# Kernel optimization log

Hardware: AMD Instinct MI355X
Metric: run time of the kernel (lower is better)

The kernel has to match this reference:

```python
import jax, jax.numpy as jnp
import numpy as np


def _pe_2d(H, W, C, dtype):
    # PositionalEncodingPermute2D: returns (C, H, W)
    ch_half = (C + 1) // 2
    inv = 1.0 / (10000.0 ** (jnp.arange(0, ch_half, 2, dtype=jnp.float32) / ch_half))
    tH = jnp.arange(H, dtype=jnp.float32)
    tW = jnp.arange(W, dtype=jnp.float32)
    sinH = tH[:, None] * inv[None, :]              # (H, ch_half//2)
    sinW = tW[:, None] * inv[None, :]              # (W, ch_half//2)
    embH = jnp.concatenate([jnp.sin(sinH), jnp.cos(sinH)], axis=-1)  # (H, ch_half)
    embW = jnp.concatenate([jnp.sin(sinW), jnp.cos(sinW)], axis=-1)  # (W, ch_half)
    E = jnp.concatenate([
        jnp.broadcast_to(embW[None, :, :], (H, W, ch_half)),
        jnp.broadcast_to(embH[:, None, :], (H, W, ch_half)),
    ], axis=-1)[..., :C]                            # (H, W, C)
    return jnp.transpose(E, (2, 0, 1)).astype(dtype)  # (C, H, W)


def setup_inputs() -> dict:
    key = jax.random.key(0)
    k0, k1, k2, k3 = jax.random.split(key, 4)
    B, C, H, W = 4, 256, 64, 64
    s = 1.0 / np.sqrt(C)  # kaiming-ish scale
    return {
        "x": jax.random.normal(k0, (B, C, H, W), dtype=jnp.float32),
        "wq": jax.random.normal(k1, (C, C), dtype=jnp.float32) * s,
        "wk": jax.random.normal(k2, (C, C), dtype=jnp.float32) * s,
        "wv": jax.random.normal(k3, (C, C), dtype=jnp.float32) * s,
    }


def reference(x, wq, wk, wv):
    B, C, H, W = x.shape
    scale = C ** (-0.5)
    x = x + _pe_2d(H, W, C, x.dtype)[None]          # (B, C, H, W)
    X = x.reshape(B, C, H * W).transpose(0, 2, 1)   # (B, N, C)
    Q = jnp.einsum('bnc,dc->bnd', X, wq)
    K = jnp.einsum('bnc,dc->bnd', X, wk)
    V = jnp.einsum('bnc,dc->bnd', X, wv)
    A = jax.nn.softmax(jnp.einsum('bnd,bmd->bnm', Q, K) * scale, axis=-1)
    Y = jnp.einsum('bnm,bmd->bnd', A, V)            # (B, N, C)
    return Y.transpose(0, 2, 1).reshape(B, C, H, W)
```

## Files before the change

### kernel.cpp

```cpp
#include <hip/hip_runtime.h>
#include <hip/hip_bf16.h>

#define BB 4
#define CC 256
#define NN 4096
#define NSPLIT 4
#define KSPLIT (NN / NSPLIT)
#define NPAIR (KSPLIT / 64)

typedef __attribute__((ext_vector_type(8))) short short8;
typedef __attribute__((ext_vector_type(4))) float floatx4;
typedef __attribute__((ext_vector_type(4))) unsigned short ushortx4;

__device__ __forceinline__ float bf2f(unsigned short u) {
  union { unsigned int i; float f; } cv; cv.i = ((unsigned int)u) << 16; return cv.f;
}
__device__ __forceinline__ unsigned short f2bf(float f) {
  union { __hip_bfloat16 h; unsigned short u; } cv; cv.h = __float2bfloat16(f); return cv.u;
}
__device__ __forceinline__ unsigned int cvtpk_bf16(float lo, float hi) {
  unsigned int r;
  asm("v_cvt_pk_bf16_f32 %0, %1, %2" : "=v"(r) : "v"(lo), "v"(hi));
  return r;
}

#define MFMA(a, b, c) __builtin_amdgcn_mfma_f32_16x16x32_bf16((a), (b), (c), 0, 0, 0)

__device__ __forceinline__ void dma16(const unsigned short* g, unsigned short* l) {
  __builtin_amdgcn_global_load_lds(
      (const __attribute__((address_space(1))) unsigned int*)g,
      (__attribute__((address_space(3))) unsigned int*)l, 16, 0, 0);
}
#define S_BARRIER __builtin_amdgcn_s_barrier()
#define MEMFENCE __asm__ volatile("" ::: "memory")

__global__ __launch_bounds__(256) void wcvt(const float* __restrict__ w0,
                                            const float* __restrict__ w1,
                                            const float* __restrict__ w2,
                                            unsigned short* __restrict__ o0,
                                            unsigned short* __restrict__ o1,
                                            unsigned short* __restrict__ o2) {
  const float* w = (blockIdx.y == 0) ? w0 : (blockIdx.y == 1) ? w1 : w2;
  unsigned short* o = (blockIdx.y == 0) ? o0 : (blockIdx.y == 1) ? o1 : o2;
  float s = (blockIdx.y == 0) ? 0.0901684400555590f : 1.0f;
  int i = (blockIdx.x * 256 + threadIdx.x) * 4;
  floatx4 v = *(const floatx4*)&w[i];
  ushortx4 p;
#pragma unroll
  for (int r = 0; r < 4; r++) p[r] = f2bf(v[r] * s);
  *(ushortx4*)&o[i] = p;
}

__global__ __launch_bounds__(256) void prep_x(const float* __restrict__ x,
                                              unsigned short* __restrict__ Xbf) {
  __shared__ float tile[32][33];
  int b = blockIdx.z;
  int n0 = blockIdx.x * 32, c0 = blockIdx.y * 32;
  int tx = threadIdx.x, ty = threadIdx.y;
#pragma unroll
  for (int i = 0; i < 4; i++) {
    int c = c0 + ty + i * 8;
    int n = n0 + tx;
    float v = x[((long)(b * CC + c)) * NN + n];
    int hh = n >> 6, ww = n & 63;
    int j = c & 63;
    float freq = exp2f(-0.2076205059304601f * (float)j);
    float arg = (float)((c < 128) ? ww : hh) * freq;
    v += (c & 64) ? cosf(arg) : sinf(arg);
    tile[ty + i * 8][tx] = v;
  }
  __syncthreads();
#pragma unroll
  for (int i = 0; i < 4; i++) {
    int n = n0 + ty + i * 8;
    int c = c0 + tx;
    Xbf[((long)(b * NN + n)) * CC + c] = f2bf(tile[tx][ty + i * 8]);
  }
}

__global__ __launch_bounds__(256, 2) void gemm_fused(const unsigned short* __restrict__ Xbf,
                                                     const unsigned short* __restrict__ Wqk,
                                                     const unsigned short* __restrict__ Wv,
                                                     unsigned short* __restrict__ QK,
                                                     unsigned short* __restrict__ Vt) {
  __shared__ alignas(16) unsigned short Af[2][8 * 512];
  __shared__ alignas(16) unsigned short Bf[2][8 * 512];
  const unsigned short *Ab, *Bb;
  unsigned short* Ob;
  long row0, col0;
  int ldo;
  int F = blockIdx.x;
  if (F < 512) {
    int b = F >> 7, r = F & 127;
    row0 = (long)(r >> 2) * 128;
    col0 = (long)(r & 3) * 128;
    Ab = Xbf + (long)b * NN * CC;
    Bb = Wqk;
    Ob = QK + (long)b * NN * 512;
    ldo = 512;
  } else {
    int F2 = F - 512;
    int b = F2 >> 6, r = F2 & 63;
    row0 = (long)(r >> 5) * 128;
    col0 = (long)(r & 31) * 128;
    Ab = Wv;
    Bb = Xbf + (long)b * NN * CC;
    Ob = Vt + (long)b * CC * NN;
    ldo = NN;
  }
  int t = threadIdx.x, wave = t >> 6, lane = t & 63, quad = lane >> 4, l15 = lane & 15;
  int wr = wave >> 1, wc = wave & 1;

  auto stage = [&](int k0, int buf) {
#pragma unroll
    for (int i = 0; i < 2; i++) {
      int fg = wave * 2 + i;
      dma16(&Ab[(row0 + fg * 16 + l15) * 256 + k0 + quad * 8], &Af[buf][fg * 512]);
      dma16(&Bb[(col0 + fg * 16 + l15) * 256 + k0 + quad * 8], &Bf[buf][fg * 512]);
    }
  };

  floatx4 acc[4][4] = {};
  stage(0, 0);
  MEMFENCE;
#pragma unroll
  for (int ki = 0; ki < 8; ki++) {
    int buf = ki & 1;
    S_BARRIER;
    MEMFENCE;
    if (ki + 1 < 8) {
      stage((ki + 1) * 32, buf ^ 1);
      MEMFENCE;
      __builtin_amdgcn_s_waitcnt(0xF74);
    } else {
      __builtin_amdgcn_s_waitcnt(0xF70);
    }
    S_BARRIER;
    MEMFENCE;
    short8 af[4], bf[4];
#pragma unroll
    for (int i = 0; i < 4; i++) {
      af[i] = *(const short8*)&Af[buf][(wr * 4 + i) * 512 + lane * 8];
      bf[i] = *(const short8*)&Bf[buf][(wc * 4 + i) * 512 + lane * 8];
    }
#pragma unroll
    for (int i = 0; i < 4; i++)
#pragma unroll
      for (int j = 0; j < 4; j++) acc[i][j] = MFMA(af[i], bf[j], acc[i][j]);
  }

#pragma unroll
  for (int i = 0; i < 4; i++)
#pragma unroll
    for (int j = 0; j < 4; j++) {
      long col = col0 + (wc * 4 + j) * 16 + l15;
#pragma unroll
      for (int r = 0; r < 4; r++) {
        long row = row0 + (wr * 4 + i) * 16 + quad * 4 + r;
        Ob[row * (long)ldo + col] = f2bf(acc[i][j][r]);
      }
    }
}

__global__ __launch_bounds__(512, 2) void attn(const unsigned short* __restrict__ QKg,
                                               const unsigned short* __restrict__ Vtg,
                                               unsigned short* __restrict__ Opart,
                                               float* __restrict__ Lp) {
  __shared__ alignas(16) unsigned short Kl[4 * 8192];
  __shared__ alignas(16) unsigned short Vl[4 * 8192];
  int F = blockIdx.x;
  int c = F & 15, sp = c & 3, b = c >> 2;
  long q0 = (long)(F >> 4) * 256;
  int t = threadIdx.x, wave = t >> 6, lane = t & 63, quad = lane >> 4, l15 = lane & 15;
  const unsigned short* Qb = QKg + (long)b * NN * 512;
  const unsigned short* Kb = Qb + 256;
  const unsigned short* Vb = Vtg + (long)b * CC * NN;

  short8 qf[2][8];
#pragma unroll
  for (int qb = 0; qb < 2; qb++) {
    long qrow = q0 + wave * 32 + qb * 16 + l15;
#pragma unroll
    for (int ks = 0; ks < 8; ks++)
      qf[qb][ks] = *(const short8*)&Qb[qrow * 512 + ks * 32 + quad * 8];
  }

  floatx4 acc[2][16] = {};
  float rs[2] = {0.f, 0.f};

  const int idx0 = (((lane >> 4) & 1) << 7) | ((lane & 15) << 2);
  const int idx1 = idx0 + 64;
  const bool lo32 = lane < 32;

  const int kbeg = sp * KSPLIT;

  auto stage_pair = [&](int p, int buf) {
#pragma unroll
    for (int tt = 0; tt < 2; tt++) {
      int m0 = kbeg + (p * 2 + tt) * 32;
      int slot = buf * 2 + tt;
#pragma unroll
      for (int st = 0; st < 2; st++) {
        int fg = st * 8 + wave;
        dma16(&Kb[(long)(m0 + st * 16 + l15) * 512 + wave * 32 + quad * 8],
              &Kl[slot * 8192 + fg * 512]);
        dma16(&Vb[(long)(fg * 16 + l15) * NN + m0 + quad * 8],
              &Vl[slot * 8192 + fg * 512]);
      }
    }
  };

  __builtin_amdgcn_s_waitcnt(0xF70);
  stage_pair(0, 0);
  MEMFENCE;

  for (int p = 0; p < NPAIR; p++) {
    int buf = p & 1;
    S_BARRIER;
    MEMFENCE;
    if (p + 1 < NPAIR) {
      stage_pair(p + 1, buf ^ 1);
      MEMFENCE;
      __builtin_amdgcn_s_waitcnt(0xF78);
    } else {
      __builtin_amdgcn_s_waitcnt(0xF70);
    }
    S_BARRIER;
    MEMFENCE;

#pragma unroll
    for (int tt = 0; tt < 2; tt++) {
      int kb = (buf * 2 + tt) * 8192;
      floatx4 s2[2][2];
      {
        floatx4 z = {0.f, 0.f, 0.f, 0.f};
        s2[0][0] = z; s2[0][1] = z; s2[1][0] = z; s2[1][1] = z;
      }
      __builtin_amdgcn_s_setprio(1);
#pragma unroll
      for (int fgk = 0; fgk < 16; fgk++) {
        short8 kf = *(const short8*)&Kl[kb + fgk * 512 + lane * 8];
        int mt = fgk >> 3, ks = fgk & 7;
        s2[0][mt] = MFMA(kf, qf[0][ks], s2[0][mt]);
        s2[1][mt] = MFMA(kf, qf[1][ks], s2[1][mt]);
      }
      __builtin_amdgcn_s_setprio(0);

      unsigned int pw[2][2][2];
#pragma unroll
      for (int qb = 0; qb < 2; qb++)
#pragma unroll
        for (int mt = 0; mt < 2; mt++) {
          float e0 = __builtin_amdgcn_exp2f(s2[qb][mt][0]);
          float e1 = __builtin_amdgcn_exp2f(s2[qb][mt][1]);
          float e2 = __builtin_amdgcn_exp2f(s2[qb][mt][2]);
          float e3 = __builtin_amdgcn_exp2f(s2[qb][mt][3]);
          rs[qb] += (e0 + e1) + (e2 + e3);
          pw[qb][mt][0] = cvtpk_bf16(e0, e1);
          pw[qb][mt][1] = cvtpk_bf16(e2, e3);
        }

      short8 pf[2];
#pragma unroll
      for (int qb = 0; qb < 2; qb++) {
        unsigned int x0 = (unsigned int)__builtin_amdgcn_ds_bpermute(idx0, (int)pw[qb][0][0]);
        unsigned int y0 = (unsigned int)__builtin_amdgcn_ds_bpermute(idx0, (int)pw[qb][1][0]);
        unsigned int x1 = (unsigned int)__builtin_amdgcn_ds_bpermute(idx0, (int)pw[qb][0][1]);
        unsigned int y1 = (unsigned int)__builtin_amdgcn_ds_bpermute(idx0, (int)pw[qb][1][1]);
        unsigned int x2 = (unsigned int)__builtin_amdgcn_ds_bpermute(idx1, (int)pw[qb][0][0]);
        unsigned int y2 = (unsigned int)__builtin_amdgcn_ds_bpermute(idx1, (int)pw[qb][1][0]);
        unsigned int x3 = (unsigned int)__builtin_amdgcn_ds_bpermute(idx1, (int)pw[qb][0][1]);
        unsigned int y3 = (unsigned int)__builtin_amdgcn_ds_bpermute(idx1, (int)pw[qb][1][1]);
        union { unsigned int u[4]; short8 s; } pk;
        pk.u[0] = lo32 ? x0 : y0;
        pk.u[1] = lo32 ? x1 : y1;
        pk.u[2] = lo32 ? x2 : y2;
        pk.u[3] = lo32 ? x3 : y3;
        pf[qb] = pk.s;
      }

      __builtin_amdgcn_s_setprio(1);
#pragma unroll
      for (int db = 0; db < 16; db++) {
        short8 vf = *(const short8*)&Vl[kb + db * 512 + lane * 8];
        acc[0][db] = MFMA(pf[0], vf, acc[0][db]);
        acc[1][db] = MFMA(pf[1], vf, acc[1][db]);
      }
      __builtin_amdgcn_s_setprio(0);
    }
  }

  unsigned short* Ob = Opart + (long)(b * NSPLIT + sp) * CC * NN;
#pragma unroll
  for (int qb = 0; qb < 2; qb++) {
    long nidx = q0 + wave * 32 + qb * 16 + quad * 4;
#pragma unroll
    for (int db = 0; db < 16; db++) {
      long d = db * 16 + l15;
      ushortx4 pk;
#pragma unroll
      for (int r = 0; r < 4; r++) pk[r] = f2bf(acc[qb][db][r]);
      *(ushortx4*)&Ob[d * NN + nidx] = pk;
    }
    float v = rs[qb];
    v += __shfl_xor(v, 16, 64);
    v += __shfl_xor(v, 32, 64);
    if (quad == 0)
      Lp[(long)(b * NSPLIT + sp) * NN + q0 + wave * 32 + qb * 16 + l15] = v;
  }
}

__global__ __launch_bounds__(256) void combine(const unsigned short* __restrict__ Op,
                                               const float* __restrict__ Lp,
                                               float* __restrict__ Out) {
  __shared__ float Wl[64];
  int b = blockIdx.z;
  int d0 = blockIdx.y * 64, n0 = blockIdx.x * 64;
  int t = threadIdx.x;
  if (t < 64) {
    int n = n0 + t;
    float L = 0.f;
#pragma unroll
    for (int s = 0; s < NSPLIT; s++) L += Lp[(long)(b * NSPLIT + s) * NN + n];
    Wl[t] = 1.0f / L;
  }
  __syncthreads();
  int tn = t & 15, td = t >> 4;
  int nb = n0 + tn * 4;
  float w[4];
#pragma unroll
  for (int r = 0; r < 4; r++) w[r] = Wl[tn * 4 + r];
#pragma unroll
  for (int dd = 0; dd < 4; dd++) {
    int d = d0 + td * 4 + dd;
    floatx4 o = {0.f, 0.f, 0.f, 0.f};
#pragma unroll
    for (int s = 0; s < NSPLIT; s++) {
      ushortx4 pv = *(const ushortx4*)&Op[((long)(b * NSPLIT + s) * CC + d) * NN + nb];
#pragma unroll
      for (int r = 0; r < 4; r++) o[r] += bf2f(pv[r]);
    }
#pragma unroll
    for (int r = 0; r < 4; r++) o[r] *= w[r];
    *(floatx4*)&Out[((long)b * CC + d) * NN + nb] = o;
  }
}

extern "C" void kernel_launch(void* const* d_in, const int* in_sizes, int n_in,
                              void* d_out, int out_size, void* d_ws, size_t ws_size,
                              hipStream_t stream) {
  const float* x = (const float*)d_in[0];
  const float* wq = (const float*)d_in[1];
  const float* wk = (const float*)d_in[2];
  const float* wv = (const float*)d_in[3];
  float* out = (float*)d_out;

  char* ws = (char*)d_ws;
  unsigned short* QKbuf = (unsigned short*)(ws);
  unsigned short* Vt = (unsigned short*)(ws + (16l << 20));
  unsigned short* Xbf = (unsigned short*)(ws + (24l << 20));
  unsigned short* Opart = (unsigned short*)(ws + (24l << 20));
  float* Lp = (float*)(ws + (56l << 20));
  unsigned short* Wqk = (unsigned short*)(ws + (57l << 20));
  unsigned short* Wv = (unsigned short*)(ws + (57l << 20) + (1 << 19));

  wcvt<<<dim3(CC * CC / 1024, 3), 256, 0, stream>>>(wq, wk, wv, Wqk, Wqk + CC * CC, Wv);
  prep_x<<<dim3(NN / 32, CC / 32, BB), dim3(32, 8), 0, stream>>>(x, Xbf);
  gemm_fused<<<dim3(768), 256, 0, stream>>>(Xbf, Wqk, Wv, QKbuf, Vt);
  attn<<<dim3(256), 512, 0, stream>>>(QKbuf, Vt, Opart, Lp);
  combine<<<dim3(NN / 64, CC / 64, BB), 256, 0, stream>>>(Opart, Lp, out);
}
```

Before: 192.8 us.

## Halve attention query tile per block and double-buffer single key tiles

The attention kernel now gives each wave 16 query rows instead of 32, so a block covers 128 queries and the grid doubles to 512 blocks. It stages one 32-key tile at a time into a two-slot buffer instead of pairs of tiles into four slots, which halves LDS use and drops the min-blocks launch bound. The intent is to cut registers and LDS per block so more blocks fit per CU and latency is hidden better. In exchange, each K/V tile loaded into LDS is reused by half as many query rows, which doubles K/V global traffic and adds barrier overhead per key tile.

Result: slower. 240.0 us (+24.5%).

```diff
diff --git a/kernel.cpp b/kernel.cpp
--- a/kernel.cpp
+++ b/kernel.cpp
@@ -6,7 +6,7 @@
 #define NN 4096
 #define NSPLIT 4
 #define KSPLIT (NN / NSPLIT)
-#define NPAIR (KSPLIT / 64)
+#define NT (KSPLIT / 32)
 
 typedef __attribute__((ext_vector_type(8))) short short8;
 typedef __attribute__((ext_vector_type(4))) float floatx4;
@@ -162,31 +162,31 @@
     }
 }
 
-__global__ __launch_bounds__(512, 2) void attn(const unsigned short* __restrict__ QKg,
-                                               const unsigned short* __restrict__ Vtg,
-                                               unsigned short* __restrict__ Opart,
-                                               float* __restrict__ Lp) {
-  __shared__ alignas(16) unsigned short Kl[4 * 8192];
-  __shared__ alignas(16) unsigned short Vl[4 * 8192];
+__global__ __launch_bounds__(512) void attn(const unsigned short* __restrict__ QKg,
+                                            const unsigned short* __restrict__ Vtg,
+                                            unsigned short* __restrict__ Opart,
+                                            float* __restrict__ Lp) {
+  __shared__ alignas(16) unsigned short Kl[2 * 8192];
+  __shared__ alignas(16) unsigned short Vl[2 * 8192];
   int F = blockIdx.x;
-  int c = F & 15, sp = c & 3, b = c >> 2;
-  long q0 = (long)(F >> 4) * 256;
+  int c = F >> 5, qt = F & 31;
+  int sp = c & 3, b = c >> 2;
+  long q0 = (long)qt * 128;
   int t = threadIdx.x, wave = t >> 6, lane = t & 63, quad = lane >> 4, l15 = lane & 15;
   const unsigned short* Qb = QKg + (long)b * NN * 512;
   const unsigned short* Kb = Qb + 256;
   const unsigned short* Vb = Vtg + (long)b * CC * NN;
 
-  short8 qf[2][8];
-#pragma unroll
-  for (int qb = 0; qb < 2; qb++) {
-    long qrow = q0 + wave * 32 + qb * 16 + l15;
+  short8 qf[8];
+  {
+    long qrow = q0 + wave * 16 + l15;
 #pragma unroll
     for (int ks = 0; ks < 8; ks++)
-      qf[qb][ks] = *(const short8*)&Qb[qrow * 512 + ks * 32 + quad * 8];
-  }
-
-  floatx4 acc[2][16] = {};
-  float rs[2] = {0.f, 0.f};
+      qf[ks] = *(const short8*)&Qb[qrow * 512 + ks * 32 + quad * 8];
+  }
+
+  floatx4 acc[16] = {};
+  float rs = 0.f;
 
   const int idx0 = (((lane >> 4) & 1) << 7) | ((lane & 15) << 2);
   const int idx1 = idx0 + 64;
@@ -194,120 +194,105 @@
 
   const int kbeg = sp * KSPLIT;
 
-  auto stage_pair = [&](int p, int buf) {
-#pragma unroll
-    for (int tt = 0; tt < 2; tt++) {
-      int m0 = kbeg + (p * 2 + tt) * 32;
-      int slot = buf * 2 + tt;
-#pragma unroll
-      for (int st = 0; st < 2; st++) {
-        int fg = st * 8 + wave;
-        dma16(&Kb[(long)(m0 + st * 16 + l15) * 512 + wave * 32 + quad * 8],
-              &Kl[slot * 8192 + fg * 512]);
-        dma16(&Vb[(long)(fg * 16 + l15) * NN + m0 + quad * 8],
-              &Vl[slot * 8192 + fg * 512]);
-      }
+  auto stageT = [&](int tt) {
+    int m0 = kbeg + tt * 32;
+    int kb = (tt & 1) * 8192;
+#pragma unroll
+    for (int st = 0; st < 2; st++) {
+      int fg = st * 8 + wave;
+      dma16(&Kb[(long)(m0 + st * 16 + l15) * 512 + wave * 32 + quad * 8],
+            &Kl[kb + fg * 512]);
+      dma16(&Vb[(long)(fg * 16 + l15) * NN + m0 + quad * 8],
+            &Vl[kb + fg * 512]);
     }
   };
 
-  __builtin_amdgcn_s_waitcnt(0xF70);
-  stage_pair(0, 0);
   MEMFENCE;
-
-  for (int p = 0; p < NPAIR; p++) {
-    int buf = p & 1;
+  __builtin_amdgcn_s_waitcnt(0x070);
+  MEMFENCE;
+  stageT(0);
+  MEMFENCE;
+
+#pragma unroll 1
+  for (int tt = 0; tt < NT; tt++) {
     S_BARRIER;
     MEMFENCE;
-    if (p + 1 < NPAIR) {
-      stage_pair(p + 1, buf ^ 1);
+    if (tt + 1 < NT) {
+      stageT(tt + 1);
       MEMFENCE;
-      __builtin_amdgcn_s_waitcnt(0xF78);
+      __builtin_amdgcn_s_waitcnt(0xF74);
     } else {
       __builtin_amdgcn_s_waitcnt(0xF70);
     }
     S_BARRIER;
     MEMFENCE;
 
-#pragma unroll
-    for (int tt = 0; tt < 2; tt++) {
-      int kb = (buf * 2 + tt) * 8192;
-      floatx4 s2[2][2];
-      {
-        floatx4 z = {0.f, 0.f, 0.f, 0.f};
-        s2[0][0] = z; s2[0][1] = z; s2[1][0] = z; s2[1][1] = z;
-      }
-      __builtin_amdgcn_s_setprio(1);
-#pragma unroll
-      for (int fgk = 0; fgk < 16; fgk++) {
-        short8 kf = *(const short8*)&Kl[kb + fgk * 512 + lane * 8];
-        int mt = fgk >> 3, ks = fgk & 7;
-        s2[0][mt] = MFMA(kf, qf[0][ks], s2[0][mt]);
-        s2[1][mt] = MFMA(kf, qf[1][ks], s2[1][mt]);
-      }
-      __builtin_amdgcn_s_setprio(0);
-
-      unsigned int pw[2][2][2];
-#pragma unroll
-      for (int qb = 0; qb < 2; qb++)
-#pragma unroll
-        for (int mt = 0; mt < 2; mt++) {
-          float e0 = __builtin_amdgcn_exp2f(s2[qb][mt][0]);
-          float e1 = __builtin_amdgcn_exp2f(s2[qb][mt][1]);
-          float e2 = __builtin_amdgcn_exp2f(s2[qb][mt][2]);
-          float e3 = __builtin_amdgcn_exp2f(s2[qb][mt][3]);
-          rs[qb] += (e0 + e1) + (e2 + e3);
-          pw[qb][mt][0] = cvtpk_bf16(e0, e1);
-          pw[qb][mt][1] = cvtpk_bf16(e2, e3);
-        }
-
-      short8 pf[2];
-#pragma unroll
-      for (int qb = 0; qb < 2; qb++) {
-        unsigned int x0 = (unsigned int)__builtin_amdgcn_ds_bpermute(idx0, (int)pw[qb][0][0]);
-        unsigned int y0 = (unsigned int)__builtin_amdgcn_ds_bpermute(idx0, (int)pw[qb][1][0]);
-        unsigned int x1 = (unsigned int)__builtin_amdgcn_ds_bpermute(idx0, (int)pw[qb][0][1]);
-        unsigned int y1 = (unsigned int)__builtin_amdgcn_ds_bpermute(idx0, (int)pw[qb][1][1]);
-        unsigned int x2 = (unsigned int)__builtin_amdgcn_ds_bpermute(idx1, (int)pw[qb][0][0]);
-        unsigned int y2 = (unsigned int)__builtin_amdgcn_ds_bpermute(idx1, (int)pw[qb][1][0]);
-        unsigned int x3 = (unsigned int)__builtin_amdgcn_ds_bpermute(idx1, (int)pw[qb][0][1]);
-        unsigned int y3 = (unsigned int)__builtin_amdgcn_ds_bpermute(idx1, (int)pw[qb][1][1]);
-        union { unsigned int u[4]; short8 s; } pk;
-        pk.u[0] = lo32 ? x0 : y0;
-        pk.u[1] = lo32 ? x1 : y1;
-        pk.u[2] = lo32 ? x2 : y2;
-        pk.u[3] = lo32 ? x3 : y3;
-        pf[qb] = pk.s;
-      }
-
-      __builtin_amdgcn_s_setprio(1);
-#pragma unroll
-      for (int db = 0; db < 16; db++) {
-        short8 vf = *(const short8*)&Vl[kb + db * 512 + lane * 8];
-        acc[0][db] = MFMA(pf[0], vf, acc[0][db]);
-        acc[1][db] = MFMA(pf[1], vf, acc[1][db]);
-      }
-      __builtin_amdgcn_s_setprio(0);
-    }
+    int kb = (tt & 1) * 8192;
+
+    floatx4 s2[2];
+    { floatx4 z = {0.f, 0.f, 0.f, 0.f}; s2[0] = z; s2[1] = z; }
+    __builtin_amdgcn_s_setprio(1);
+#pragma unroll
+    for (int fgk = 0; fgk < 16; fgk++) {
+      short8 kf = *(const short8*)&Kl[kb + fgk * 512 + lane * 8];
+      s2[fgk >> 3] = MFMA(kf, qf[fgk & 7], s2[fgk >> 3]);
+    }
+    __builtin_amdgcn_s_setprio(0);
+
+    unsigned int pw[2][2];
+#pragma unroll
+    for (int mt = 0; mt < 2; mt++) {
+      float e0 = __builtin_amdgcn_exp2f(s2[mt][0]);
+      float e1 = __builtin_amdgcn_exp2f(s2[mt][1]);
+      float e2 = __builtin_amdgcn_exp2f(s2[mt][2]);
+      float e3 = __builtin_amdgcn_exp2f(s2[mt][3]);
+      rs += (e0 + e1) + (e2 + e3);
+      pw[mt][0] = cvtpk_bf16(e0, e1);
+      pw[mt][1] = cvtpk_bf16(e2, e3);
+    }
+
+    short8 pf;
+    {
+      unsigned int x0 = (unsigned int)__builtin_amdgcn_ds_bpermute(idx0, (int)pw[0][0]);
+      unsigned int y0 = (unsigned int)__builtin_amdgcn_ds_bpermute(idx0, (int)pw[1][0]);
+      unsigned int x1 = (unsigned int)__builtin_amdgcn_ds_bpermute(idx0, (int)pw[0][1]);
+      unsigned int y1 = (unsigned int)__builtin_amdgcn_ds_bpermute(idx0, (int)pw[1][1]);
+      unsigned int x2 = (unsigned int)__builtin_amdgcn_ds_bpermute(idx1, (int)pw[0][0]);
+      unsigned int y2 = (unsigned int)__builtin_amdgcn_ds_bpermute(idx1, (int)pw[1][0]);
+      unsigned int x3 = (unsigned int)__builtin_amdgcn_ds_bpermute(idx1, (int)pw[0][1]);
+      unsigned int y3 = (unsigned int)__builtin_amdgcn_ds_bpermute(idx1, (int)pw[1][1]);
+      union { unsigned int u[4]; short8 s; } pk;
+      pk.u[0] = lo32 ? x0 : y0;
+      pk.u[1] = lo32 ? x1 : y1;
+      pk.u[2] = lo32 ? x2 : y2;
+      pk.u[3] = lo32 ? x3 : y3;
+      pf = pk.s;
+    }
+
+    __builtin_amdgcn_s_setprio(1);
+#pragma unroll
+    for (int db = 0; db < 16; db++) {
+      short8 vf = *(const short8*)&Vl[kb + db * 512 + lane * 8];
+      acc[db] = MFMA(pf, vf, acc[db]);
+    }
+    __builtin_amdgcn_s_setprio(0);
   }
 
   unsigned short* Ob = Opart + (long)(b * NSPLIT + sp) * CC * NN;
-#pragma unroll
-  for (int qb = 0; qb < 2; qb++) {
-    long nidx = q0 + wave * 32 + qb * 16 + quad * 4;
-#pragma unroll
-    for (int db = 0; db < 16; db++) {
-      long d = db * 16 + l15;
-      ushortx4 pk;
-#pragma unroll
-      for (int r = 0; r < 4; r++) pk[r] = f2bf(acc[qb][db][r]);
-      *(ushortx4*)&Ob[d * NN + nidx] = pk;
-    }
-    float v = rs[qb];
-    v += __shfl_xor(v, 16, 64);
-    v += __shfl_xor(v, 32, 64);
-    if (quad == 0)
-      Lp[(long)(b * NSPLIT + sp) * NN + q0 + wave * 32 + qb * 16 + l15] = v;
-  }
+  long nidx = q0 + wave * 16 + quad * 4;
+#pragma unroll
+  for (int db = 0; db < 16; db++) {
+    long d = db * 16 + l15;
+    ushortx4 pk;
+#pragma unroll
+    for (int r = 0; r < 4; r++) pk[r] = f2bf(acc[db][r]);
+    *(ushortx4*)&Ob[d * NN + nidx] = pk;
+  }
+  float v = rs;
+  v += __shfl_xor(v, 16, 64);
+  v += __shfl_xor(v, 32, 64);
+  if (quad == 0)
+    Lp[(long)(b * NSPLIT + sp) * NN + q0 + wave * 16 + l15] = v;
 }
 
 __global__ __launch_bounds__(256) void combine(const unsigned short* __restrict__ Op,
@@ -367,6 +352,6 @@
   wcvt<<<dim3(CC * CC / 1024, 3), 256, 0, stream>>>(wq, wk, wv, Wqk, Wqk + CC * CC, Wv);
   prep_x<<<dim3(NN / 32, CC / 32, BB), dim3(32, 8), 0, stream>>>(x, Xbf);
   gemm_fused<<<dim3(768), 256, 0, stream>>>(Xbf, Wqk, Wv, QKbuf, Vt);
-  attn<<<dim3(256), 512, 0, stream>>>(QKbuf, Vt, Opart, Lp);
+  attn<<<dim3(512), 512, 0, stream>>>(QKbuf, Vt, Opart, Lp);
   combine<<<dim3(NN / 64, CC / 64, BB), 256, 0, stream>>>(Opart, Lp, out);
 }
```
